# Kernel optimization log

Measured on AMD Instinct MI355X. Metric: run time of the kernel, lower is better.

Reference implementation:

```python
import jax, jax.numpy as jnp
import numpy as np

B, NIN, M = 4, 4096, 16384
CIN, COUT = 256, 128
EPS_BN = 1e-5


def _mlp(x, w, b, g, beta, rm, rv):
    # x: (B, Cin, N); w: (Cout, Cin) -- Conv1d kernel_size=1
    y = jnp.einsum('oi,bin->bon', w, x) + b[:, None]
    y = g[:, None] * (y - rm[:, None]) / jnp.sqrt(rv[:, None] + EPS_BN) + beta[:, None]
    return jax.nn.relu(y)


def setup_inputs() -> dict:
    key = jax.random.key(0)
    ks = jax.random.split(key, 12)
    inp = {
        'rgb': jax.random.normal(ks[0], (B, CIN, NIN), jnp.float32),
        'xyzin': jax.random.normal(ks[1], (B, NIN, 3), jnp.float32),
        'xyzout': jax.random.normal(ks[2], (B, M, 3), jnp.float32),
        'w1': jax.random.normal(ks[3], (COUT, CIN), jnp.float32) * (1.0 / np.sqrt(CIN)),
        'b1': jnp.zeros((COUT,), jnp.float32),
        'g1': jnp.ones((COUT,), jnp.float32),
        'beta1': jnp.zeros((COUT,), jnp.float32),
        'rm1': jnp.zeros((COUT,), jnp.float32),
        'rv1': jnp.ones((COUT,), jnp.float32),
        'w2': jax.random.normal(ks[4], (COUT, COUT), jnp.float32) * (1.0 / np.sqrt(COUT)),
        'b2': jnp.zeros((COUT,), jnp.float32),
        'g2': jnp.ones((COUT,), jnp.float32),
        'beta2': jnp.zeros((COUT,), jnp.float32),
        'rm2': jnp.zeros((COUT,), jnp.float32),
        'rv2': jnp.ones((COUT,), jnp.float32),
        'w3': jax.random.normal(ks[5], (COUT, COUT), jnp.float32) * (1.0 / np.sqrt(COUT)),
        'b3': jnp.zeros((COUT,), jnp.float32),
        'g3': jnp.zeros((COUT,), jnp.float32) + 1.0,
        'beta3': jnp.zeros((COUT,), jnp.float32),
        'rm3': jnp.zeros((COUT,), jnp.float32),
        'rv3': jnp.ones((COUT,), jnp.float32),
    }
    return inp


def reference(rgb, xyzin, xyzout,
              w1, b1, g1, beta1, rm1, rv1,
              w2, b2, g2, beta2, rm2, rv2,
              w3, b3, g3, beta3, rm3, rv3):
    # 3 pointwise MLP blocks (Conv1d k=1 + BN + ReLU)
    feat = _mlp(rgb, w1, b1, g1, beta1, rm1, rv1)
    feat = _mlp(feat, w2, b2, g2, beta2, rm2, rv2)
    feat = _mlp(feat, w3, b3, g3, beta3, rm3, rv3)  # (B, COUT, NIN)

    # squared pairwise distances (B, M, NIN), clamped like the torch code:
    # get_dists clamps <0 to 1e-7 then sqrt; forward then squares -> clamped d^2
    d2 = (jnp.sum(xyzout * xyzout, -1)[:, :, None]
          + jnp.sum(xyzin * xyzin, -1)[:, None, :]
          - 2.0 * jnp.einsum('bmc,bnc->bmn', xyzout, xyzin))
    d2 = jnp.where(d2 < 0, jnp.float32(1e-7), d2)

    # top-3 smallest distances (== first 3 of full ascending sort)
    neg_vals, idx = jax.lax.top_k(-d2, 3)  # (B, M, 3)
    wv = 1.0 / (-neg_vals)
    wv = wv / jnp.sum(wv, -1, keepdims=True)

    # gather neighbor features: feat^T is (B, NIN, COUT)
    featT = jnp.transpose(feat, (0, 2, 1))
    nb = jnp.take_along_axis(featT, idx.reshape(B, M * 3, 1), axis=1)
    nb = nb.reshape(B, M, 3, COUT)

    out = jnp.einsum('bmk,bmkc->bmc', wv, nb)  # weighted interpolation
    return jnp.transpose(out, (0, 2, 1))  # (B, COUT, M)
```

## Files before the change

### kernel.cpp

```cpp
#include <hip/hip_runtime.h>
#include <hip/hip_bf16.h>
#include <cstdint>
#include <cstddef>

constexpr int BB   = 4;
constexpr int NIN  = 4096;
constexpr int MM   = 16384;
constexpr int CIN  = 256;
constexpr int COUT = 128;
constexpr float EPSBN = 1e-5f;

__global__ __launch_bounds__(256) void prep_kernel(
    const float* __restrict__ w1, const float* __restrict__ w2, const float* __restrict__ w3,
    const float* __restrict__ b1, const float* __restrict__ g1, const float* __restrict__ be1,
    const float* __restrict__ rm1, const float* __restrict__ rv1,
    const float* __restrict__ b2, const float* __restrict__ g2, const float* __restrict__ be2,
    const float* __restrict__ rm2, const float* __restrict__ rv2,
    const float* __restrict__ b3, const float* __restrict__ g3, const float* __restrict__ be3,
    const float* __restrict__ rm3, const float* __restrict__ rv3,
    const float* __restrict__ xyzin,
    float* __restrict__ WT1, float* __restrict__ WT2, float* __restrict__ WT3,
    float* __restrict__ st, float4* __restrict__ packed)
{
    int tid  = blockIdx.x * blockDim.x + threadIdx.x;
    int nthr = gridDim.x * blockDim.x;

    for (int i = tid; i < CIN * COUT; i += nthr)
        WT1[i] = w1[(i & 127) * CIN + (i >> 7)];
    for (int i = tid; i < COUT * COUT; i += nthr)
        WT2[i] = w2[(i & 127) * COUT + (i >> 7)];
    for (int i = tid; i < COUT * COUT; i += nthr)
        WT3[i] = w3[(i & 127) * COUT + (i >> 7)];

    for (int i = tid; i < 3 * COUT; i += nthr) {
        int l = i >> 7, o = i & 127;
        const float* bb = (l == 0) ? b1 : (l == 1) ? b2 : b3;
        const float* gg = (l == 0) ? g1 : (l == 1) ? g2 : g3;
        const float* be = (l == 0) ? be1 : (l == 1) ? be2 : be3;
        const float* rm = (l == 0) ? rm1 : (l == 1) ? rm2 : rm3;
        const float* rv = (l == 0) ? rv1 : (l == 1) ? rv2 : rv3;
        float s = gg[o] / sqrtf(rv[o] + EPSBN);
        st[l * 256 + o]       = s;
        st[l * 256 + 128 + o] = s * (bb[o] - rm[o]) + be[o];
    }

    for (int i = tid; i < BB * NIN; i += nthr) {
        float x = xyzin[i * 3 + 0], y = xyzin[i * 3 + 1], z = xyzin[i * 3 + 2];
        float sn = __fadd_rn(__fadd_rn(__fmul_rn(x, x), __fmul_rn(y, y)), __fmul_rn(z, z));
        packed[i] = make_float4(x, y, z, sn);
    }
}

template <int CI, bool TOUT>
__global__ __launch_bounds__(256) void mlp_kernel(
    const float* __restrict__ in, const float* __restrict__ WT,
    const float* __restrict__ svec, const float* __restrict__ tvec,
    float* __restrict__ out)
{
    __shared__ float Xs[32][32];
    __shared__ float Ws[32][128];

    int blk = blockIdx.x;
    int b   = blk >> 7;
    int n0  = (blk & 127) * 32;
    int t   = threadIdx.x;
    int og  = t & 31;
    int ng  = t >> 5;

    float acc[4][4] = {};
    const float* inb = in + (size_t)b * CI * NIN;

    for (int k0 = 0; k0 < CI; k0 += 32) {
        __syncthreads();
        {
            int r = t >> 3, c = (t & 7) * 4;
            *(float4*)&Xs[r][c] = *(const float4*)&inb[(size_t)(k0 + r) * NIN + n0 + c];
        }
        #pragma unroll
        for (int r = 0; r < 4; ++r) {
            int e = (r * 256 + t) * 4;
            *(float4*)&Ws[0][e] = *(const float4*)&WT[(size_t)k0 * 128 + e];
        }
        __syncthreads();
        #pragma unroll
        for (int kk = 0; kk < 32; ++kk) {
            float w[4], xv[4];
            *(float4*)w  = *(const float4*)&Ws[kk][og * 4];
            *(float4*)xv = *(const float4*)&Xs[kk][ng * 4];
            #pragma unroll
            for (int oi = 0; oi < 4; ++oi)
                #pragma unroll
                for (int j = 0; j < 4; ++j)
                    acc[oi][j] = fmaf(w[oi], xv[j], acc[oi][j]);
        }
    }

    #pragma unroll
    for (int oi = 0; oi < 4; ++oi) {
        float s  = svec[og * 4 + oi];
        float tt = tvec[og * 4 + oi];
        #pragma unroll
        for (int j = 0; j < 4; ++j)
            acc[oi][j] = fmaxf(fmaf(s, acc[oi][j], tt), 0.0f);
    }

    if (TOUT) {
        #pragma unroll
        for (int j = 0; j < 4; ++j) {
            int n = n0 + ng * 4 + j;
            float4 v = make_float4(acc[0][j], acc[1][j], acc[2][j], acc[3][j]);
            *(float4*)&out[((size_t)(b * NIN + n)) * COUT + og * 4] = v;
        }
    } else {
        #pragma unroll
        for (int oi = 0; oi < 4; ++oi) {
            int o = og * 4 + oi;
            float4 v = make_float4(acc[oi][0], acc[oi][1], acc[oi][2], acc[oi][3]);
            *(float4*)&out[((size_t)b * COUT + o) * NIN + n0 + ng * 4] = v;
        }
    }
}

__global__ __launch_bounds__(512) void knn_kernel(
    const float4* __restrict__ packed, const float* __restrict__ xyzout,
    float* __restrict__ topw, int* __restrict__ topi)
{
    __shared__ float PD[8][64][3];
    __shared__ int   PI[8][64][3];

    int b  = blockIdx.y;
    int m0 = blockIdx.x * 64;
    int t  = threadIdx.x;
    int ml = t & 63, q = t >> 6;
    int m  = m0 + ml;

    size_t ob = ((size_t)b * MM + m) * 3;
    float x = xyzout[ob], y = xyzout[ob + 1], z = xyzout[ob + 2];
    float sm = __fadd_rn(__fadd_rn(__fmul_rn(x, x), __fmul_rn(y, y)), __fmul_rn(z, z));

    int qs = __builtin_amdgcn_readfirstlane(q);
    int nbase = qs * 512;
    const float4* pb = packed + (size_t)b * NIN + nbase;

    float e0 = 3.402823466e38f, e1 = 3.402823466e38f, e2 = 3.402823466e38f;
    int j0 = 0, j1 = 0, j2 = 0;

    for (int i0 = 0; i0 < 512; i0 += 8) {
        float4 pv[8];
        #pragma unroll
        for (int u = 0; u < 8; ++u) pv[u] = pb[i0 + u];
        #pragma unroll
        for (int u = 0; u < 8; ++u) {
            float4 p = pv[u];
            float dot = __fadd_rn(__fadd_rn(__fmul_rn(x, p.x), __fmul_rn(y, p.y)), __fmul_rn(z, p.z));
            float d   = __fsub_rn(__fadd_rn(sm, p.w), __fmul_rn(2.0f, dot));
            int   n   = nbase + i0 + u;
            bool lt0 = d < e0, lt1 = d < e1, lt2 = d < e2;
            float ne0 = fminf(e0, d);
            float ne1 = __builtin_amdgcn_fmed3f(d, e0, e1);
            float ne2 = __builtin_amdgcn_fmed3f(d, e1, e2);
            int nj2 = lt2 ? (lt1 ? j1 : n) : j2;
            int nj1 = lt1 ? (lt0 ? j0 : n) : j1;
            j0 = lt0 ? n : j0;
            e0 = ne0; e1 = ne1; e2 = ne2;
            j1 = nj1; j2 = nj2;
        }
    }

    PD[q][ml][0] = e0; PD[q][ml][1] = e1; PD[q][ml][2] = e2;
    PI[q][ml][0] = j0; PI[q][ml][1] = j1; PI[q][ml][2] = j2;
    __syncthreads();

    if (t < 64) {
        float f0 = 3.402823466e38f, f1 = 3.402823466e38f, f2 = 3.402823466e38f;
        int i0 = 0, i1 = 0, i2 = 0;
        #pragma unroll
        for (int qq = 0; qq < 8; ++qq) {
            #pragma unroll
            for (int k = 0; k < 3; ++k) {
                float d = PD[qq][t][k];
                int   n = PI[qq][t][k];
                bool lt0 = d < f0, lt1 = d < f1, lt2 = d < f2;
                float ne1 = __builtin_amdgcn_fmed3f(d, f0, f1);
                float ne2 = __builtin_amdgcn_fmed3f(d, f1, f2);
                int nj2 = lt2 ? (lt1 ? i1 : n) : i2;
                int nj1 = lt1 ? (lt0 ? i0 : n) : i1;
                f0 = fminf(f0, d);  i0 = lt0 ? n : i0;
                f1 = ne1; i1 = nj1;
                f2 = ne2; i2 = nj2;
            }
        }
        f0 = fmaxf(f0, 1e-7f); f1 = fmaxf(f1, 1e-7f); f2 = fmaxf(f2, 1e-7f);
        float iv0 = 1.0f / f0, iv1 = 1.0f / f1, iv2 = 1.0f / f2;
        float s = iv0 + iv1 + iv2;
        size_t wb = ((size_t)b * MM + m0 + t) * 3;
        topw[wb + 0] = iv0 / s; topw[wb + 1] = iv1 / s; topw[wb + 2] = iv2 / s;
        topi[wb + 0] = i0;      topi[wb + 1] = i1;      topi[wb + 2] = i2;
    }
}

__global__ __launch_bounds__(256) void interp_kernel(
    const float* __restrict__ featT, const float* __restrict__ topw,
    const int* __restrict__ topi, float* __restrict__ out)
{
    __shared__ float G[32][388];
    __shared__ float Wl[32][4];

    int b  = blockIdx.y;
    int m0 = blockIdx.x * 32;
    int t  = threadIdx.x;

    if (t < 96) {
        int mm = t / 3, k = t - (t / 3) * 3;
        Wl[mm][k] = topw[((size_t)b * MM + m0 + mm) * 3 + k];
    }
    int lane = t & 31, r8 = t >> 5;
    #pragma unroll
    for (int pass = 0; pass < 12; ++pass) {
        int r  = pass * 8 + r8;
        int mm = r / 3, k = r - (r / 3) * 3;
        int idx = topi[((size_t)b * MM + m0 + mm) * 3 + k];
        const float4 v = *(const float4*)&featT[((size_t)(b * NIN + idx)) * COUT + lane * 4];
        *(float4*)&G[mm][k * 128 + lane * 4] = v;
    }
    __syncthreads();

    int m  = t & 31;
    int obq = (t >> 5) * 16;
    float w0 = Wl[m][0], w1 = Wl[m][1], w2 = Wl[m][2];
    const float* Gm = &G[m][0];
    size_t outbase = ((size_t)b * COUT) * MM + m0 + m;
    #pragma unroll
    for (int oi = 0; oi < 16; ++oi) {
        int o = obq + oi;
        float v = w0 * Gm[o] + w1 * Gm[128 + o] + w2 * Gm[256 + o];
        out[outbase + (size_t)o * MM] = v;
    }
}

extern "C" void kernel_launch(void* const* d_in, const int* in_sizes, int n_in,
                              void* d_out, int out_size, void* d_ws, size_t ws_size,
                              hipStream_t stream)
{
    const float* rgb    = (const float*)d_in[0];
    const float* xyzin  = (const float*)d_in[1];
    const float* xyzout = (const float*)d_in[2];
    const float* w1  = (const float*)d_in[3];
    const float* b1  = (const float*)d_in[4];
    const float* g1  = (const float*)d_in[5];
    const float* be1 = (const float*)d_in[6];
    const float* rm1 = (const float*)d_in[7];
    const float* rv1 = (const float*)d_in[8];
    const float* w2  = (const float*)d_in[9];
    const float* b2  = (const float*)d_in[10];
    const float* g2  = (const float*)d_in[11];
    const float* be2 = (const float*)d_in[12];
    const float* rm2 = (const float*)d_in[13];
    const float* rv2 = (const float*)d_in[14];
    const float* w3  = (const float*)d_in[15];
    const float* b3  = (const float*)d_in[16];
    const float* g3  = (const float*)d_in[17];
    const float* be3 = (const float*)d_in[18];
    const float* rm3 = (const float*)d_in[19];
    const float* rv3 = (const float*)d_in[20];
    float* out = (float*)d_out;

    float* ws   = (float*)d_ws;
    float* WT1  = ws;
    float* WT2  = WT1 + 32768;
    float* WT3  = WT2 + 16384;
    float* st   = WT3 + 16384;
    float4* packed = (float4*)(st + 768);
    float* featA = st + 768 + 65536;
    float* featB = featA + 2097152;
    float* topw  = featB + 2097152;
    int*   topi  = (int*)(topw + 196608);

    prep_kernel<<<256, 256, 0, stream>>>(w1, w2, w3,
        b1, g1, be1, rm1, rv1,
        b2, g2, be2, rm2, rv2,
        b3, g3, be3, rm3, rv3,
        xyzin, WT1, WT2, WT3, st, packed);

    mlp_kernel<CIN, false><<<dim3(BB * (NIN / 32)), 256, 0, stream>>>(
        rgb, WT1, st + 0, st + 128, featA);
    mlp_kernel<COUT, false><<<dim3(BB * (NIN / 32)), 256, 0, stream>>>(
        featA, WT2, st + 256, st + 384, featB);
    mlp_kernel<COUT, true><<<dim3(BB * (NIN / 32)), 256, 0, stream>>>(
        featB, WT3, st + 512, st + 640, featA);

    knn_kernel<<<dim3(MM / 64, BB), 512, 0, stream>>>(packed, xyzout, topw, topi);

    interp_kernel<<<dim3(MM / 32, BB), 256, 0, stream>>>(featA, topw, topi, out);
}
```

Measured before the change: 283.3 us.

## Fuse MLP layers 2 and 3 and add wave-level early skip in KNN

Layers 2 and 3 of the pointwise MLP now run in one kernel that keeps the intermediate activations in shared memory. This removes a launch and the global write and read of one feature tensor. The KNN inner loop folds the factor of 2 into the packed input coordinates and skips the top-3 update when no lane in the wavefront improves its third-best distance. This cuts the per-candidate ALU work in the dominant KNN loop, at the cost of a wave-uniform branch. Scaling by 2 is exact in floating point, so the distances computed should not change.

New measurement: 262.2 us. 1.08x faster.

```diff
diff --git a/kernel.cpp b/kernel.cpp
--- a/kernel.cpp
+++ b/kernel.cpp
@@ -47,7 +47,7 @@
     for (int i = tid; i < BB * NIN; i += nthr) {
         float x = xyzin[i * 3 + 0], y = xyzin[i * 3 + 1], z = xyzin[i * 3 + 2];
         float sn = __fadd_rn(__fadd_rn(__fmul_rn(x, x), __fmul_rn(y, y)), __fmul_rn(z, z));
-        packed[i] = make_float4(x, y, z, sn);
+        packed[i] = make_float4(2.0f * x, 2.0f * y, 2.0f * z, sn);
     }
 }
 
@@ -121,6 +121,101 @@
     }
 }
 
+__global__ __launch_bounds__(256) void mlp23_kernel(
+    const float* __restrict__ in,
+    const float* __restrict__ WT2, const float* __restrict__ WT3,
+    const float* __restrict__ s2, const float* __restrict__ t2,
+    const float* __restrict__ s3, const float* __restrict__ t3,
+    float* __restrict__ featT)
+{
+    __shared__ float X[128][36];
+    __shared__ float Y[128][36];
+    __shared__ float Ws[32][128];
+
+    int blk = blockIdx.x;
+    int b   = blk >> 7;
+    int n0  = (blk & 127) * 32;
+    int t   = threadIdx.x;
+    int og  = t & 31;
+    int ng  = t >> 5;
+
+    const float* inb = in + (size_t)b * COUT * NIN;
+    #pragma unroll
+    for (int r4 = 0; r4 < 4; ++r4) {
+        int e   = r4 * 256 + t;
+        int row = e >> 3, c = (e & 7) * 4;
+        *(float4*)&X[row][c] = *(const float4*)&inb[(size_t)row * NIN + n0 + c];
+    }
+
+    float acc[4][4] = {};
+    for (int k0 = 0; k0 < COUT; k0 += 32) {
+        __syncthreads();
+        #pragma unroll
+        for (int r = 0; r < 4; ++r) {
+            int e = (r * 256 + t) * 4;
+            *(float4*)&Ws[0][e] = *(const float4*)&WT2[(size_t)k0 * 128 + e];
+        }
+        __syncthreads();
+        #pragma unroll
+        for (int kk = 0; kk < 32; ++kk) {
+            float w[4], xv[4];
+            *(float4*)w  = *(const float4*)&Ws[kk][og * 4];
+            *(float4*)xv = *(const float4*)&X[k0 + kk][ng * 4];
+            #pragma unroll
+            for (int oi = 0; oi < 4; ++oi)
+                #pragma unroll
+                for (int j = 0; j < 4; ++j)
+                    acc[oi][j] = fmaf(w[oi], xv[j], acc[oi][j]);
+        }
+    }
+    #pragma unroll
+    for (int oi = 0; oi < 4; ++oi) {
+        float s = s2[og * 4 + oi], tt = t2[og * 4 + oi];
+        float4 v;
+        v.x = fmaxf(fmaf(s, acc[oi][0], tt), 0.0f);
+        v.y = fmaxf(fmaf(s, acc[oi][1], tt), 0.0f);
+        v.z = fmaxf(fmaf(s, acc[oi][2], tt), 0.0f);
+        v.w = fmaxf(fmaf(s, acc[oi][3], tt), 0.0f);
+        *(float4*)&Y[og * 4 + oi][ng * 4] = v;
+    }
+    __syncthreads();
+
+    float acc2[4][4] = {};
+    for (int k0 = 0; k0 < COUT; k0 += 32) {
+        __syncthreads();
+        #pragma unroll
+        for (int r = 0; r < 4; ++r) {
+            int e = (r * 256 + t) * 4;
+            *(float4*)&Ws[0][e] = *(const float4*)&WT3[(size_t)k0 * 128 + e];
+        }
+        __syncthreads();
+        #pragma unroll
+        for (int kk = 0; kk < 32; ++kk) {
+            float w[4], xv[4];
+            *(float4*)w  = *(const float4*)&Ws[kk][og * 4];
+            *(float4*)xv = *(const float4*)&Y[k0 + kk][ng * 4];
+            #pragma unroll
+            for (int oi = 0; oi < 4; ++oi)
+                #pragma unroll
+                for (int j = 0; j < 4; ++j)
+                    acc2[oi][j] = fmaf(w[oi], xv[j], acc2[oi][j]);
+        }
+    }
+    #pragma unroll
+    for (int oi = 0; oi < 4; ++oi) {
+        float s = s3[og * 4 + oi], tt = t3[og * 4 + oi];
+        #pragma unroll
+        for (int j = 0; j < 4; ++j)
+            acc2[oi][j] = fmaxf(fmaf(s, acc2[oi][j], tt), 0.0f);
+    }
+    #pragma unroll
+    for (int j = 0; j < 4; ++j) {
+        int n = n0 + ng * 4 + j;
+        float4 v = make_float4(acc2[0][j], acc2[1][j], acc2[2][j], acc2[3][j]);
+        *(float4*)&featT[((size_t)(b * NIN + n)) * COUT + og * 4] = v;
+    }
+}
+
 __global__ __launch_bounds__(512) void knn_kernel(
     const float4* __restrict__ packed, const float* __restrict__ xyzout,
     float* __restrict__ topw, int* __restrict__ topi)
@@ -152,18 +247,19 @@
         #pragma unroll
         for (int u = 0; u < 8; ++u) {
             float4 p = pv[u];
-            float dot = __fadd_rn(__fadd_rn(__fmul_rn(x, p.x), __fmul_rn(y, p.y)), __fmul_rn(z, p.z));
-            float d   = __fsub_rn(__fadd_rn(sm, p.w), __fmul_rn(2.0f, dot));
-            int   n   = nbase + i0 + u;
-            bool lt0 = d < e0, lt1 = d < e1, lt2 = d < e2;
-            float ne0 = fminf(e0, d);
-            float ne1 = __builtin_amdgcn_fmed3f(d, e0, e1);
-            float ne2 = __builtin_amdgcn_fmed3f(d, e1, e2);
-            int nj2 = lt2 ? (lt1 ? j1 : n) : j2;
-            int nj1 = lt1 ? (lt0 ? j0 : n) : j1;
-            j0 = lt0 ? n : j0;
-            e0 = ne0; e1 = ne1; e2 = ne2;
-            j1 = nj1; j2 = nj2;
+            float dot2 = __fadd_rn(__fadd_rn(__fmul_rn(x, p.x), __fmul_rn(y, p.y)), __fmul_rn(z, p.z));
+            float d    = __fsub_rn(__fadd_rn(sm, p.w), dot2);
+            bool lt2 = d < e2;
+            if (__any(lt2)) {
+                int n = nbase + i0 + u;
+                bool lt0 = d < e0, lt1 = d < e1;
+                j2 = lt2 ? (lt1 ? j1 : n) : j2;
+                j1 = lt1 ? (lt0 ? j0 : n) : j1;
+                j0 = lt0 ? n : j0;
+                e2 = __builtin_amdgcn_fmed3f(d, e1, e2);
+                e1 = __builtin_amdgcn_fmed3f(d, e0, e1);
+                e0 = fminf(e0, d);
+            }
         }
     }
 
@@ -181,13 +277,12 @@
                 float d = PD[qq][t][k];
                 int   n = PI[qq][t][k];
                 bool lt0 = d < f0, lt1 = d < f1, lt2 = d < f2;
-                float ne1 = __builtin_amdgcn_fmed3f(d, f0, f1);
-                float ne2 = __builtin_amdgcn_fmed3f(d, f1, f2);
-                int nj2 = lt2 ? (lt1 ? i1 : n) : i2;
-                int nj1 = lt1 ? (lt0 ? i0 : n) : i1;
-                f0 = fminf(f0, d);  i0 = lt0 ? n : i0;
-                f1 = ne1; i1 = nj1;
-                f2 = ne2; i2 = nj2;
+                i2 = lt2 ? (lt1 ? i1 : n) : i2;
+                i1 = lt1 ? (lt0 ? i0 : n) : i1;
+                i0 = lt0 ? n : i0;
+                f2 = __builtin_amdgcn_fmed3f(d, f1, f2);
+                f1 = __builtin_amdgcn_fmed3f(d, f0, f1);
+                f0 = fminf(f0, d);
             }
         }
         f0 = fmaxf(f0, 1e-7f); f1 = fmaxf(f1, 1e-7f); f2 = fmaxf(f2, 1e-7f);
@@ -284,12 +379,11 @@
 
     mlp_kernel<CIN, false><<<dim3(BB * (NIN / 32)), 256, 0, stream>>>(
         rgb, WT1, st + 0, st + 128, featA);
-    mlp_kernel<COUT, false><<<dim3(BB * (NIN / 32)), 256, 0, stream>>>(
-        featA, WT2, st + 256, st + 384, featB);
-    mlp_kernel<COUT, true><<<dim3(BB * (NIN / 32)), 256, 0, stream>>>(
-        featB, WT3, st + 512, st + 640, featA);
+
+    mlp23_kernel<<<dim3(BB * (NIN / 32)), 256, 0, stream>>>(
+        featA, WT2, WT3, st + 256, st + 384, st + 512, st + 640, featB);
 
     knn_kernel<<<dim3(MM / 64, BB), 512, 0, stream>>>(packed, xyzout, topw, topi);
 
-    interp_kernel<<<dim3(MM / 32, BB), 256, 0, stream>>>(featA, topw, topi, out);
-}
+    interp_kernel<<<dim3(MM / 32, BB), 256, 0, stream>>>(featB, topw, topi, out);
+}
```
